# Performance work log

Hardware: AMD Instinct MI355X
Metric: run time of the kernel (lower is better)

The kernel has to match this reference:

```python
import jax, jax.numpy as jnp
import numpy as np

N_FRAG = 1_000_000
CELL_N = 1000
GENE_N = 500
N_GENES = 5000
H = 100   # hidden dims
E = 100   # embedding dims


def setup_inputs() -> dict:
    key = jax.random.key(0)
    ks = jax.random.split(key, 16)
    coords = jax.random.randint(ks[0], (N_FRAG, 2), 0, 1000, dtype=jnp.int64 if jax.config.jax_enable_x64 else jnp.int32)
    cxg_ix = jnp.sort(jax.random.randint(ks[1], (N_FRAG,), 0, CELL_N * GENE_N))
    gene_ix = jax.random.randint(ks[2], (GENE_N,), 0, N_GENES)
    stdv_in = 1.0 / np.sqrt(2)
    stdv_h = 1.0 / np.sqrt(H)
    u = lambda k, shape, s: jax.random.uniform(k, shape, jnp.float32, -s, s)
    W0 = u(ks[3], (2, H), stdv_in); b0 = u(ks[4], (H,), stdv_in)
    W1 = u(ks[5], (H, H), stdv_h); b1 = u(ks[6], (H,), stdv_h)
    W2 = u(ks[7], (H, H), stdv_h); b2 = u(ks[8], (H,), stdv_h)
    W3 = u(ks[9], (H, E), stdv_h); b3 = u(ks[10], (E,), stdv_h)
    weight1 = u(ks[11], (N_GENES, E), stdv_h / 100.0)  # torch init: stdv/100
    bias1 = jax.random.normal(ks[12], (N_GENES,), jnp.float32)  # mean gene expression
    return {
        "fragment_coordinates": coords,
        "fragment_cellxgene_ix": cxg_ix,
        "cell_n": CELL_N,
        "gene_n": GENE_N,
        "gene_ix": gene_ix,
        "W0": W0, "b0": b0, "W1": W1, "b1": b1,
        "W2": W2, "b2": b2, "W3": W3, "b3": b3,
        "weight1": weight1, "bias1": bias1,
    }


def reference(fragment_coordinates, fragment_cellxgene_ix, cell_n, gene_n, gene_ix,
              W0, b0, W1, b1, W2, b2, W3, b3, weight1, bias1):
    # FragmentEmbedder: 4-layer MLP on scaled coordinates
    x = fragment_coordinates.astype(jnp.float32) / 1000.0          # [F, 2]
    h = jax.nn.relu(x @ W0 + b0)
    h = jax.nn.relu(h @ W1 + b1)
    h = jax.nn.relu(h @ W2 + b2)
    emb = h @ W3 + b3                                              # [F, E]
    # EmbeddingGenePooler: segment-sum into cell x gene bins
    pooled = jax.ops.segment_sum(emb, fragment_cellxgene_ix,
                                 num_segments=cell_n * gene_n)     # [C*G, E]
    cg = pooled.reshape(cell_n, gene_n, -1)                        # [C, G, E]
    # EmbeddingToExpression: gene-specific weighted sum + bias
    out = jnp.einsum('cge,ge->cg', cg, weight1[gene_ix]) + bias1[gene_ix]
    return out
```

## Files before the change

kernel.cpp:

```cpp
#include <hip/hip_runtime.h>
#include <hip/hip_bf16.h>

typedef __attribute__((ext_vector_type(4))) short s16x4;
typedef __attribute__((ext_vector_type(4))) float f32x4;

#define GENE_N     500
#define WG_STRIDE  112
#define WSW_FRAGS  154
#define WG_OFF_BYTES 81920

__device__ __forceinline__ unsigned short f2bf(float x){
  __hip_bfloat16 h = __float2bfloat16(x);
  return *reinterpret_cast<unsigned short*>(&h);
}

__device__ __forceinline__ f32x4 mfma16(s16x4 a, s16x4 b, f32x4 c){
#if __has_builtin(__builtin_amdgcn_mfma_f32_16x16x16bf16_1k)
  return __builtin_amdgcn_mfma_f32_16x16x16bf16_1k(a, b, c, 0, 0, 0);
#else
  asm volatile("v_mfma_f32_16x16x16_bf16 %0, %1, %2, %0"
               : "+v"(c) : "v"(a), "v"(b));
  return c;
#endif
}

__global__ void init_out(const int* __restrict__ gene_ix,
                         const float* __restrict__ bias1,
                         float* __restrict__ out, int n){
  int t = blockIdx.x*blockDim.x + threadIdx.x;
  if (t < n) out[t] = bias1[gene_ix[t % GENE_N]];
}

__global__ void prep_weights(const float* __restrict__ W0, const float* __restrict__ b0,
                             const float* __restrict__ W1, const float* __restrict__ b1,
                             const float* __restrict__ W2, const float* __restrict__ b2,
                             const float* __restrict__ W3, const float* __restrict__ b3,
                             unsigned short* __restrict__ wsW){
  int t = blockIdx.x*blockDim.x + threadIdx.x;
  if (t >= WSW_FRAGS*64) return;
  int fr = t >> 6, lane = t & 63;
  int grp = lane >> 4, row = lane & 15;
  int L, m, kt;
  if (fr < 7){ L = 0; m = fr; kt = 0; }
  else { int r = fr - 7; L = 1 + r/49; r %= 49; m = r/7; kt = r%7; }
  int up = m*16 + row;
  const float* W = (L==0)?W0:(L==1)?W1:(L==2)?W2:W3;
  const float* B = (L==0)?b0:(L==1)?b1:(L==2)?b2:b3;
  #pragma unroll
  for (int i = 0; i < 4; ++i){
    float val = 0.f;
    if (up < 100){
      int k = kt*16 + grp*4 + i;
      if (L == 0){
        if (k < 2)        val = W[k*100 + up];
        else if (k == 2)  val = B[up];
      } else {
        if (k < 100)      val = W[k*100 + up];
        else if (k == 100) val = B[up];
      }
    }
    wsW[t*4 + i] = f2bf(val);
  }
}

__global__ void prep_wg(const int* __restrict__ gene_ix,
                        const float* __restrict__ weight1,
                        float* __restrict__ wg){
  int t = blockIdx.x*blockDim.x + threadIdx.x;
  if (t >= GENE_N*WG_STRIDE) return;
  int g = t / WG_STRIDE, e = t % WG_STRIDE;
  wg[t] = (e < 100) ? weight1[gene_ix[g]*100 + e] : 0.f;
}

#define RELUPACK(GDST, INJECT)                                         \
  _Pragma("unroll")                                                    \
  for (int m = 0; m < 7; ++m){                                         \
    float r0 = fmaxf(acc[m][0], 0.f);                                  \
    float r1 = fmaxf(acc[m][1], 0.f);                                  \
    float r2 = fmaxf(acc[m][2], 0.f);                                  \
    float r3 = fmaxf(acc[m][3], 0.f);                                  \
    if (INJECT && m == 6 && grp == 1) r0 = 1.0f;  \
    GDST[m][0] = (short)f2bf(r0);                                      \
    GDST[m][1] = (short)f2bf(r1);                                      \
    GDST[m][2] = (short)f2bf(r2);                                      \
    GDST[m][3] = (short)f2bf(r3);                                      \
  }

__global__ __launch_bounds__(64, 1)
void frag_mlp_pool(const int* __restrict__ coords, const int* __restrict__ cxg,
                   const unsigned short* __restrict__ wsW,
                   const float* __restrict__ wg,
                   float* __restrict__ out, int nfrag, int ntiles){
  const int lane = threadIdx.x & 63;
  const int grp = lane >> 4, row = lane & 15;
  const s16x4* wf = (const s16x4*)wsW;

  s16x4 A0[7], A1[49], A2[49], A3[49];
  #pragma unroll
  for (int i = 0; i < 7;  ++i) A0[i] = wf[i*64 + lane];
  #pragma unroll
  for (int i = 0; i < 49; ++i) A1[i] = wf[(7   + i)*64 + lane];
  #pragma unroll
  for (int i = 0; i < 49; ++i) A2[i] = wf[(56  + i)*64 + lane];
  #pragma unroll
  for (int i = 0; i < 49; ++i) A3[i] = wf[(105 + i)*64 + lane];

  const f32x4 zero = {0.f, 0.f, 0.f, 0.f};

  for (int tile = blockIdx.x; tile < ntiles; tile += gridDim.x){
    int fbase = tile*16;
    int f  = fbase + row;
    int fc = (f < nfrag) ? f : (nfrag - 1);

    int2 cd = ((const int2*)coords)[fc];
    s16x4 bx;
    bx[0] = (short)f2bf((float)cd.x * 1e-3f);
    bx[1] = (short)f2bf((float)cd.y * 1e-3f);
    bx[2] = (short)0x3F80;
    bx[3] = 0;

    f32x4 acc[7];
    #pragma unroll
    for (int m = 0; m < 7; ++m) acc[m] = mfma16(A0[m], bx, zero);

    s16x4 g[7];
    RELUPACK(g, 1)

    #pragma unroll
    for (int m = 0; m < 7; ++m){
      f32x4 a = zero;
      #pragma unroll
      for (int kt = 0; kt < 7; ++kt) a = mfma16(A1[m*7 + kt], g[kt], a);
      acc[m] = a;
    }
    RELUPACK(g, 1)

    #pragma unroll
    for (int m = 0; m < 7; ++m){
      f32x4 a = zero;
      #pragma unroll
      for (int kt = 0; kt < 7; ++kt) a = mfma16(A2[m*7 + kt], g[kt], a);
      acc[m] = a;
    }
    RELUPACK(g, 1)

    #pragma unroll
    for (int m = 0; m < 7; ++m){
      f32x4 a = zero;
      #pragma unroll
      for (int kt = 0; kt < 7; ++kt) a = mfma16(A3[m*7 + kt], g[kt], a);
      acc[m] = a;
    }

    int cxgv = cxg[fc];
    int gbin = cxgv % GENE_N;
    const float* wrow = wg + gbin*WG_STRIDE + grp*4;
    float s = 0.f;
    #pragma unroll
    for (int m = 0; m < 7; ++m){
      float4 w = *(const float4*)(wrow + m*16);
      s += acc[m][0]*w.x + acc[m][1]*w.y + acc[m][2]*w.z + acc[m][3]*w.w;
    }
    s += __shfl_xor(s, 16);
    s += __shfl_xor(s, 32);
    if (lane < 16 && f < nfrag) atomicAdd(out + cxgv, s);
  }
}

extern "C" void kernel_launch(void* const* d_in, const int* in_sizes, int n_in,
                              void* d_out, int out_size, void* d_ws, size_t ws_size,
                              hipStream_t stream){
  const int* coords  = (const int*)d_in[0];
  const int* cxg     = (const int*)d_in[1];
  const int* gene_ix = (const int*)d_in[4];
  const float* W0 = (const float*)d_in[5];
  const float* b0 = (const float*)d_in[6];
  const float* W1 = (const float*)d_in[7];
  const float* b1 = (const float*)d_in[8];
  const float* W2 = (const float*)d_in[9];
  const float* b2 = (const float*)d_in[10];
  const float* W3 = (const float*)d_in[11];
  const float* b3 = (const float*)d_in[12];
  const float* weight1 = (const float*)d_in[13];
  const float* bias1   = (const float*)d_in[14];

  int nfrag  = in_sizes[1];
  int ntiles = (nfrag + 15) / 16;

  unsigned short* wsW = (unsigned short*)d_ws;
  float* wg = (float*)((char*)d_ws + WG_OFF_BYTES);
  float* out = (float*)d_out;

  hipLaunchKernelGGL(init_out, dim3((out_size + 255)/256), dim3(256), 0, stream,
                     gene_ix, bias1, out, out_size);
  hipLaunchKernelGGL(prep_weights, dim3((WSW_FRAGS*64 + 255)/256), dim3(256), 0, stream,
                     W0, b0, W1, b1, W2, b2, W3, b3, wsW);
  hipLaunchKernelGGL(prep_wg, dim3((GENE_N*WG_STRIDE + 255)/256), dim3(256), 0, stream,
                     gene_ix, weight1, wg);
  hipLaunchKernelGGL(frag_mlp_pool, dim3(1024), dim3(64), 0, stream,
                     coords, cxg, wsW, wg, out, nfrag, ntiles);
}
```

Baseline: 198.5 us.

## Interleave two fragment tiles per iteration and prefetch next inputs

Each wave now handles two 16-fragment tiles per loop iteration. The MFMA layers of one tile are interleaved with the ReLU/bf16 packing of the other, so the dependent MFMA chains of the two tiles can overlap. Coordinates and cell-gene indices for the next pair are loaded one iteration early to hide global load latency. The cost is more accumulator and packed registers on top of the roughly 150 weight fragments already held in VGPRs, which risks spilling at one wave per SIMD.

```diff
diff --git a/kernel.cpp b/kernel.cpp
--- a/kernel.cpp
+++ b/kernel.cpp
@@ -72,19 +72,63 @@
   wg[t] = (e < 100) ? weight1[gene_ix[g]*100 + e] : 0.f;
 }
 
-#define RELUPACK(GDST, INJECT)                                         \
-  _Pragma("unroll")                                                    \
-  for (int m = 0; m < 7; ++m){                                         \
-    float r0 = fmaxf(acc[m][0], 0.f);                                  \
-    float r1 = fmaxf(acc[m][1], 0.f);                                  \
-    float r2 = fmaxf(acc[m][2], 0.f);                                  \
-    float r3 = fmaxf(acc[m][3], 0.f);                                  \
-    if (INJECT && m == 6 && grp == 1) r0 = 1.0f;  \
-    GDST[m][0] = (short)f2bf(r0);                                      \
-    GDST[m][1] = (short)f2bf(r1);                                      \
-    GDST[m][2] = (short)f2bf(r2);                                      \
-    GDST[m][3] = (short)f2bf(r3);                                      \
-  }
+
+__device__ __forceinline__ void mfma_layer(const s16x4* __restrict__ A,
+                                           const s16x4* __restrict__ g,
+                                           f32x4* __restrict__ acc){
+  const f32x4 zero = {0.f,0.f,0.f,0.f};
+  #pragma unroll
+  for (int m = 0; m < 7; ++m){
+    f32x4 a = zero;
+    #pragma unroll
+    for (int kt = 0; kt < 7; ++kt) a = mfma16(A[m*7 + kt], g[kt], a);
+    acc[m] = a;
+  }
+}
+
+__device__ __forceinline__ void pack_relu(const f32x4* __restrict__ acc,
+                                          s16x4* __restrict__ g, int grp){
+  #pragma unroll
+  for (int m = 0; m < 7; ++m){
+    float r0 = fmaxf(acc[m][0], 0.f);
+    float r1 = fmaxf(acc[m][1], 0.f);
+    float r2 = fmaxf(acc[m][2], 0.f);
+    float r3 = fmaxf(acc[m][3], 0.f);
+    if (m == 6 && grp == 1) r0 = 1.0f;
+    s16x4 v;
+    v[0] = (short)f2bf(r0);
+    v[1] = (short)f2bf(r1);
+    v[2] = (short)f2bf(r2);
+    v[3] = (short)f2bf(r3);
+    g[m] = v;
+  }
+}
+
+__device__ __forceinline__ void epi_store(const f32x4* __restrict__ acc,
+                                          const float* __restrict__ wg,
+                                          int grp, int lane, int f, int nfrag,
+                                          int cxgv, float* __restrict__ out){
+  int gbin = cxgv % GENE_N;
+  const float* wrow = wg + gbin*WG_STRIDE + grp*4;
+  float s = 0.f;
+  #pragma unroll
+  for (int m = 0; m < 7; ++m){
+    float4 w = *(const float4*)(wrow + m*16);
+    s += acc[m][0]*w.x + acc[m][1]*w.y + acc[m][2]*w.z + acc[m][3]*w.w;
+  }
+  s += __shfl_xor(s, 16);
+  s += __shfl_xor(s, 32);
+  if (lane < 16 && f < nfrag) atomicAdd(out + cxgv, s);
+}
+
+__device__ __forceinline__ s16x4 build_bx(int2 cd){
+  s16x4 v;
+  v[0] = (short)f2bf((float)cd.x * 1e-3f);
+  v[1] = (short)f2bf((float)cd.y * 1e-3f);
+  v[2] = (short)0x3F80;
+  v[3] = 0;
+  return v;
+}
 
 __global__ __launch_bounds__(64, 1)
 void frag_mlp_pool(const int* __restrict__ coords, const int* __restrict__ cxg,
@@ -105,65 +149,52 @@
   #pragma unroll
   for (int i = 0; i < 49; ++i) A3[i] = wf[(105 + i)*64 + lane];
 
-  const f32x4 zero = {0.f, 0.f, 0.f, 0.f};
-
-  for (int tile = blockIdx.x; tile < ntiles; tile += gridDim.x){
-    int fbase = tile*16;
-    int f  = fbase + row;
-    int fc = (f < nfrag) ? f : (nfrag - 1);
-
-    int2 cd = ((const int2*)coords)[fc];
-    s16x4 bx;
-    bx[0] = (short)f2bf((float)cd.x * 1e-3f);
-    bx[1] = (short)f2bf((float)cd.y * 1e-3f);
-    bx[2] = (short)0x3F80;
-    bx[3] = 0;
-
-    f32x4 acc[7];
+  const f32x4 zero = {0.f,0.f,0.f,0.f};
+  const int npairs = (ntiles + 1) >> 1;
+  const int lastf = nfrag - 1;
+
+  int p0 = blockIdx.x;
+  int fA = p0*32 + row, fB = p0*32 + 16 + row;
+  int cA = (fA < nfrag) ? fA : lastf;
+  int cB = (fB < nfrag) ? fB : lastf;
+  int2 cdA = ((const int2*)coords)[cA];
+  int2 cdB = ((const int2*)coords)[cB];
+  int  xgA = cxg[cA];
+  int  xgB = cxg[cB];
+
+  for (int p = p0; p < npairs; p += gridDim.x){
+    int f0 = p*32 + row, f1 = p*32 + 16 + row;
+    int2 cd0 = cdA, cd1 = cdB;
+    int  xg0 = xgA, xg1 = xgB;
+
+    int pn = p + gridDim.x;
+    int fAn = pn*32 + row, fBn = pn*32 + 16 + row;
+    int cAn = (fAn < nfrag) ? fAn : lastf;
+    int cBn = (fBn < nfrag) ? fBn : lastf;
+    cdA = ((const int2*)coords)[cAn];
+    cdB = ((const int2*)coords)[cBn];
+    xgA = cxg[cAn];
+    xgB = cxg[cBn];
+
+    s16x4 bx0 = build_bx(cd0);
+    s16x4 bx1 = build_bx(cd1);
+    f32x4 acc0[7], acc1[7];
     #pragma unroll
-    for (int m = 0; m < 7; ++m) acc[m] = mfma16(A0[m], bx, zero);
-
-    s16x4 g[7];
-    RELUPACK(g, 1)
-
+    for (int m = 0; m < 7; ++m) acc0[m] = mfma16(A0[m], bx0, zero);
     #pragma unroll
-    for (int m = 0; m < 7; ++m){
-      f32x4 a = zero;
-      #pragma unroll
-      for (int kt = 0; kt < 7; ++kt) a = mfma16(A1[m*7 + kt], g[kt], a);
-      acc[m] = a;
-    }
-    RELUPACK(g, 1)
-
-    #pragma unroll
-    for (int m = 0; m < 7; ++m){
-      f32x4 a = zero;
-      #pragma unroll
-      for (int kt = 0; kt < 7; ++kt) a = mfma16(A2[m*7 + kt], g[kt], a);
-      acc[m] = a;
-    }
-    RELUPACK(g, 1)
-
-    #pragma unroll
-    for (int m = 0; m < 7; ++m){
-      f32x4 a = zero;
-      #pragma unroll
-      for (int kt = 0; kt < 7; ++kt) a = mfma16(A3[m*7 + kt], g[kt], a);
-      acc[m] = a;
-    }
-
-    int cxgv = cxg[fc];
-    int gbin = cxgv % GENE_N;
-    const float* wrow = wg + gbin*WG_STRIDE + grp*4;
-    float s = 0.f;
-    #pragma unroll
-    for (int m = 0; m < 7; ++m){
-      float4 w = *(const float4*)(wrow + m*16);
-      s += acc[m][0]*w.x + acc[m][1]*w.y + acc[m][2]*w.z + acc[m][3]*w.w;
-    }
-    s += __shfl_xor(s, 16);
-    s += __shfl_xor(s, 32);
-    if (lane < 16 && f < nfrag) atomicAdd(out + cxgv, s);
+    for (int m = 0; m < 7; ++m) acc1[m] = mfma16(A0[m], bx1, zero);
+
+    s16x4 g0[7], g1[7];
+    pack_relu(acc0, g0, grp);
+    mfma_layer(A1, g0, acc0);   pack_relu(acc1, g1, grp);
+    mfma_layer(A1, g1, acc1);   pack_relu(acc0, g0, grp);
+    mfma_layer(A2, g0, acc0);   pack_relu(acc1, g1, grp);
+    mfma_layer(A2, g1, acc1);   pack_relu(acc0, g0, grp);
+    mfma_layer(A3, g0, acc0);   pack_relu(acc1, g1, grp);
+    mfma_layer(A3, g1, acc1);
+
+    epi_store(acc0, wg, grp, lane, f0, nfrag, xg0, out);
+    epi_store(acc1, wg, grp, lane, f1, nfrag, xg1, out);
   }
 }
 
```

Measured after the change: 181.0 us. 1.1x faster.
